# Optimization experiments

Measured on AMD Instinct MI355X. Metric: run time of the kernel, lower is better.

Reference implementation:

```python
import jax, jax.numpy as jnp
import numpy as np
from jax import lax

# SoftDTW constants from module-level `sdtw = SoftDTW(use_cuda=False, gamma=0.01, warp=134.4)`
GAMMA = 0.01
WARP = 134.4
BIG = 1e9        # finite stand-in for inf boundary (grad-safe; exp(-BIG/GAMMA) underflows to exactly 0)
MASK_INF = 100000.0
# loss alphas (config.loss.*)
KL_ALPHA = 1.0
KL_FWD_ALPHA = 1.0
GEN_ALPHA = 1.0
GEN_E2E_ALPHA = 1.0
FEAT_ALPHA = 2.0
DUR_ALPHA = 1.0
PITCH_ALPHA = 1.0
MEL_ALPHA = 45.0


def soft_dtw(D):
    """Soft-DTW with warp penalty (NaturalSpeech variant).
    D: [b, n, m] cost matrix. Returns [b] soft-DTW values R[n-1, m-1] of
      R[i,j] = D[i,j] + softmin_gamma(R[i-1,j-1], R[i-1,j]+warp, R[i,j-1]+warp)
    computed over anti-diagonals (wavefront) so each scan step is vectorized.
    """
    b, n, m = D.shape
    K = n + m - 1
    i_idx = jnp.arange(n)
    ks = jnp.arange(K)

    def pack(k):  # pack anti-diagonal k of D, indexed by row i
        j = k - i_idx
        v = (j >= 0) & (j < m)
        return jnp.where(v[None, :], D[:, i_idx, jnp.clip(j, 0, m - 1)], 0.0), v

    Dd, Vd = jax.vmap(pack)(ks)  # Dd: [K, b, n], Vd: [K, n]
    init = jnp.full((b, n), BIG, dtype=D.dtype)

    def step(carry, xs):
        r1, r2 = carry  # previous diag (k-1) and diag (k-2), indexed by row i
        dk, v, k = xs
        # diagonal predecessor (i-1, j-1): on diag k-2 at row i-1; (−1,−1) boundary = 0 only at k==0
        first = jnp.where(k == 0, 0.0, BIG).astype(D.dtype)
        r_diag = jnp.concatenate([jnp.broadcast_to(first, (b, 1)), r2[:, :-1]], axis=1)
        # up predecessor (i-1, j): diag k-1, row i-1
        r_up = jnp.concatenate([jnp.full((b, 1), BIG, dtype=D.dtype), r1[:, :-1]], axis=1)
        # left predecessor (i, j-1): diag k-1, row i
        stacked = jnp.stack([-r_diag, -(r_up + WARP), -(r1 + WARP)]) / GAMMA
        smin = -GAMMA * jax.nn.logsumexp(stacked, axis=0)
        r_new = jnp.where(v[None, :], dk + smin, BIG)
        return (r_new, r1), None

    (rf, _), _ = lax.scan(step, (init, init), (Dd, Vd, ks))
    return rf[:, n - 1]  # cell (n-1, m-1) lies on the last diagonal at row n-1


def kl_matrix(z, lq, m, lp):
    """kl[b,p,q] = sum_h lp - lq - 0.5 + 0.5*(z-m)^2*exp(-2lp); rows (m,lp) [b,h,P], cols (z,lq) [b,h,Q]."""
    h = m.shape[1]
    a = jnp.exp(-2.0 * lp)  # [b,h,P]
    quad = (jnp.einsum('bhp,bhq->bpq', a, z * z)
            - 2.0 * jnp.einsum('bhp,bhq->bpq', a * m, z)
            + jnp.sum(a * m * m, axis=1)[:, :, None])
    return jnp.sum(lp, axis=1)[:, :, None] - jnp.sum(lq, axis=1)[:, None, :] - 0.5 * h + 0.5 * quad


def kl_loss_sdtw(z, lq, m, lp, p_mask, q_mask):
    kl = kl_matrix(z, lq, m, lp)
    kl = jnp.pad(kl, ((0, 0), (0, 1), (0, 1)))
    pmf = jnp.pad(p_mask.astype(jnp.float32), ((0, 0), (0, 1)))
    qmf = jnp.pad(q_mask.astype(jnp.float32), ((0, 0), (0, 1)))
    pb, qb = pmf.astype(bool), qmf.astype(bool)
    kl = jnp.where(pb[:, :, None] ^ qb[:, None, :], MASK_INF, kl)
    kl = jnp.where((~pb[:, :, None]) & (~qb[:, None, :]), 0.0, kl)
    return soft_dtw(kl).sum() / pmf.sum()


def setup_inputs() -> dict:
    key = jax.random.key(0)
    ks = jax.random.split(key, 16)
    B, H, T = 8, 192, 400
    d = {
        'mel_slice': jax.random.normal(ks[0], (B, 80, T), jnp.float32),
        'mel_slice_hat': jax.random.normal(ks[1], (B, 80, T), jnp.float32),
        'scores_disc_fake': jax.random.normal(ks[2], (6, B, T), jnp.float32),
        'scores_disc_fake_e2e': jax.random.normal(ks[3], (6, B, T), jnp.float32),
        'feats_disc_real': jax.random.normal(ks[4], (30, B, 128, T), jnp.float32),
        'feats_disc_fake': jax.random.normal(ks[5], (30, B, 128, T), jnp.float32),
        'duration_loss': jax.random.uniform(ks[6], (1,), jnp.float32),
        'pitch_loss': jax.random.uniform(ks[7], (1,), jnp.float32),
        'z_p': jax.random.normal(ks[8], (B, H, T), jnp.float32),
        'm_p': jax.random.normal(ks[9], (B, H, T), jnp.float32),
        'logs_p': jax.random.normal(ks[10], (B, H, T), jnp.float32),
        'z_q': jax.random.normal(ks[11], (B, H, T), jnp.float32),
        'm_q': jax.random.normal(ks[12], (B, H, T), jnp.float32),
        'logs_q': jax.random.normal(ks[13], (B, H, T), jnp.float32),
        'p_mask': jnp.ones((B, T), jnp.int32),
        'z_mask': jnp.ones((B, T), jnp.int32),
    }
    return d


def reference(mel_slice, mel_slice_hat, scores_disc_fake, scores_disc_fake_e2e,
              feats_disc_real, feats_disc_fake, duration_loss, pitch_loss,
              z_p, m_p, logs_p, z_q, m_q, logs_q, p_mask, z_mask):
    # generator losses: sum over discriminator maps of mean((1 - s)^2)
    loss_gen = jnp.mean((1.0 - scores_disc_fake) ** 2, axis=(1, 2)).sum() * GEN_ALPHA
    loss_gen_e2e = jnp.mean((1.0 - scores_disc_fake_e2e) ** 2, axis=(1, 2)).sum() * GEN_E2E_ALPHA
    # feature matching: 2 * sum over feature maps of mean|real.detach() - fake|
    fr = lax.stop_gradient(feats_disc_real)
    loss_fm = 2.0 * jnp.mean(jnp.abs(fr - feats_disc_fake), axis=(1, 2, 3)).sum() * FEAT_ALPHA
    loss_mel = jnp.mean(jnp.abs(mel_slice - mel_slice_hat)) * MEL_ALPHA
    loss_dur = jnp.sum(duration_loss) * DUR_ALPHA
    loss_pitch = jnp.sum(pitch_loss) * PITCH_ALPHA
    # soft-DTW KL (both directions)
    loss_kl = kl_loss_sdtw(z_p, logs_q, m_p, logs_p, p_mask, z_mask) * KL_ALPHA
    loss_kl_fwd = kl_loss_sdtw(z_q, logs_p, m_q, logs_q, z_mask, p_mask) * KL_FWD_ALPHA
    total = loss_gen + loss_gen_e2e + loss_fm + loss_mel + loss_dur + loss_pitch + loss_kl + loss_kl_fwd
    return jnp.stack([loss_gen, loss_gen_e2e, loss_fm, loss_mel, loss_dur,
                      loss_pitch, loss_kl, loss_kl_fwd, total])
```

## Files before the change

### kernel.cpp

```cpp
#include <hip/hip_runtime.h>
#include <math.h>

#define BIGV      1e9f
#define WARP_PEN  134.4f
#define MASK_INF_C 100000.0f

#define B   8
#define H   192
#define T   400
#define NP  401
#define NPROB 16
#define TSLAB 166464
#define SBLOCKS 768

typedef float f32x4 __attribute__((ext_vector_type(4)));

#define SLOT_OFF 16
#define LSP_OFF 160
#define LSQ_OFF (160 + B*T)
#define C1P_OFF (160 + 2*B*T)
#define C1Q_OFF (160 + 3*B*T)
#define DMAT_OFF (160 + 4*B*T)

__device__ __forceinline__ int diag_len(int s) { return (s <= 50) ? s + 1 : 101 - s; }
__device__ __forceinline__ int diag_i0 (int s) { return (s <= 50) ? 0 : s - 50; }
__device__ __forceinline__ int diag_Cs (int s) {
    return (s <= 51) ? s * (s + 1) / 2 : 2601 - (101 - s) * (102 - s) / 2;
}

__device__ __forceinline__ float wave_shr1(float src, float fill) {
    int r = __builtin_amdgcn_update_dpp(__float_as_int(fill), __float_as_int(src),
                                        0x138 , 0xf, 0xf, false);
    return __int_as_float(r);
}

__global__ __launch_bounds__(256)
void colsum(const float* __restrict__ logs_p, const float* __restrict__ m_p,
            const float* __restrict__ logs_q, const float* __restrict__ m_q,
            float* __restrict__ ws) {
    int b = blockIdx.x / 7;
    int lane = threadIdx.x & 63;
    int hq = threadIdx.x >> 6;
    int t = (blockIdx.x % 7) * 64 + lane;
    __shared__ float part[4][4][64];
    float lp_s = 0.f, lq_s = 0.f, c1p = 0.f, c1q = 0.f;
    if (t < T) {
        int base = b*H*T + hq*48*T + t;
        const float* LP = logs_p + base;
        const float* MP = m_p   + base;
        const float* LQ = logs_q + base;
        const float* MQ = m_q   + base;
#pragma unroll 4
        for (int h = 0; h < 48; ++h) {
            float lp = LP[h*T], mp = MP[h*T];
            float lq = LQ[h*T], mq = MQ[h*T];
            lp_s += lp;
            lq_s += lq;
            c1p += __expf(-2.f*lp) * mp * mp;
            c1q += __expf(-2.f*lq) * mq * mq;
        }
    }
    part[hq][0][lane] = lp_s;
    part[hq][1][lane] = lq_s;
    part[hq][2][lane] = c1p;
    part[hq][3][lane] = c1q;
    __syncthreads();
    if (hq == 0 && t < T) {
        float a0 = part[0][0][lane] + part[1][0][lane] + part[2][0][lane] + part[3][0][lane];
        float a1 = part[0][1][lane] + part[1][1][lane] + part[2][1][lane] + part[3][1][lane];
        float a2 = part[0][2][lane] + part[1][2][lane] + part[2][2][lane] + part[3][2][lane];
        float a3 = part[0][3][lane] + part[1][3][lane] + part[2][3][lane] + part[3][3][lane];
        ws[LSP_OFF + b*T + t] = a0;
        ws[LSQ_OFF + b*T + t] = a1;
        ws[C1P_OFF + b*T + t] = a2;
        ws[C1Q_OFF + b*T + t] = a3;
    }
}

#define TILE 64
#define KH 32
__global__ __launch_bounds__(256)
void kl_gemm(const float* __restrict__ z_p, const float* __restrict__ m_p,
             const float* __restrict__ logs_p,
             const float* __restrict__ z_q, const float* __restrict__ m_q,
             const float* __restrict__ logs_q,
             const int* __restrict__ p_mask, const int* __restrict__ z_mask,
             float* __restrict__ ws) {
    int prob = blockIdx.y;
    int dir = prob >> 3, b = prob & 7;
    int tp = blockIdx.x / 7, tq = blockIdx.x % 7;
    int p0 = tp * TILE, q0 = tq * TILE;

    const float* lp_arr = dir ? logs_q : logs_p;
    const float* m_arr  = dir ? m_q    : m_p;
    const float* z_arr  = dir ? z_q    : z_p;
    const float* Lp = ws + (dir ? LSQ_OFF : LSP_OFF) + b*T;
    const float* Lq = ws + (dir ? LSP_OFF : LSQ_OFF) + b*T;
    const float* C1 = ws + (dir ? C1Q_OFF : C1P_OFF) + b*T;
    const int* rmask = dir ? z_mask : p_mask;
    const int* cmask = dir ? p_mask : z_mask;

    __shared__ __align__(16) float As [KH][TILE+4];
    __shared__ __align__(16) float AMs[KH][TILE+4];
    __shared__ __align__(16) float Zs [KH][TILE+4];
    __shared__ __align__(16) float Z2s[KH][TILE+4];

    int tid = threadIdx.x;
    int tx = tid & 15, ty = tid >> 4;

    float acc1[4][4] = {{0.f}}, acc2[4][4] = {{0.f}};

    const float* lpB = lp_arr + b*H*T;
    const float* mB  = m_arr  + b*H*T;
    const float* zB  = z_arr  + b*H*T;

    for (int h0 = 0; h0 < H; h0 += KH) {
        for (int e = tid; e < KH*TILE; e += 256) {
            int hh = e >> 6, tt = e & 63;
            int pg = p0 + tt; if (pg > T-1) pg = T-1;
            int qg = q0 + tt; if (qg > T-1) qg = T-1;
            float lp = lpB[(h0+hh)*T + pg];
            float mv = mB [(h0+hh)*T + pg];
            float a  = __expf(-2.f*lp);
            As [hh][tt] = a;
            AMs[hh][tt] = a * mv;
            float zv = zB[(h0+hh)*T + qg];
            Zs [hh][tt] = zv;
            Z2s[hh][tt] = zv * zv;
        }
        __syncthreads();
#pragma unroll 8
        for (int hh = 0; hh < KH; ++hh) {
            const float4 av  = *(const float4*)(&As [hh][ty*4]);
            const float4 amv = *(const float4*)(&AMs[hh][ty*4]);
            const float4 zv  = *(const float4*)(&Zs [hh][tx*4]);
            const float4 z2v = *(const float4*)(&Z2s[hh][tx*4]);
            const float pa[4]  = {av.x, av.y, av.z, av.w};
            const float pam[4] = {amv.x, amv.y, amv.z, amv.w};
            const float qz[4]  = {zv.x, zv.y, zv.z, zv.w};
            const float qz2[4] = {z2v.x, z2v.y, z2v.z, z2v.w};
#pragma unroll
            for (int ii = 0; ii < 4; ++ii)
#pragma unroll
                for (int jj = 0; jj < 4; ++jj) {
                    acc1[ii][jj] = fmaf(pa[ii],  qz2[jj], acc1[ii][jj]);
                    acc2[ii][jj] = fmaf(pam[ii], qz[jj],  acc2[ii][jj]);
                }
        }
        __syncthreads();
    }

    float* Dm = ws + DMAT_OFF + (size_t)prob * TSLAB;
#pragma unroll
    for (int ii = 0; ii < 4; ++ii) {
        int p = p0 + ty*4 + ii;
        if (p > NP-1) continue;
        int pc = p < T ? p : T-1;
        float lpv = Lp[pc];
        float c1v = C1[pc];
        bool pmv = (p < T) && (rmask[b*T + p] != 0);
#pragma unroll
        for (int jj = 0; jj < 4; ++jj) {
            int q = q0 + tx*4 + jj;
            if (q > NP-1) continue;
            int qc = q < T ? q : T-1;
            bool qmv = (q < T) && (cmask[b*T + q] != 0);
            float val = lpv - Lq[qc] - 0.5f*(float)H
                      + 0.5f*(acc1[ii][jj] - 2.f*acc2[ii][jj] + c1v);
            float outv = (pmv != qmv) ? MASK_INF_C : ((!pmv && !qmv) ? 0.f : val);
            int I8 = p >> 3, J8 = q >> 3, sdg = I8 + J8;
            int len = diag_len(sdg), i0 = diag_i0(sdg), Cs = diag_Cs(sdg);
            int k = (p & 7) * 2 + ((q & 7) >> 2);
            int off = Cs*64 + (k*len + (I8 - i0))*4 + (q & 3);
            Dm[off] = outv;
        }
    }
}

__global__ __launch_bounds__(256)
void fused_dtw_scalar(const float* __restrict__ Dd, float* __restrict__ acc,
                      const float* __restrict__ mel, const float* __restrict__ melh,
                      const float* __restrict__ sg,  const float* __restrict__ se,
                      const float* __restrict__ fr,  const float* __restrict__ ff,
                      const int* __restrict__ pm,    const int* __restrict__ zm) {
    if (blockIdx.x < NPROB) {
        if (threadIdx.x >= 64) return;
        int prob = blockIdx.x;
        int lane = threadIdx.x;
        const float* Dp = Dd + (size_t)prob * TSLAB;

        float brow[8], browW[8], rightraw[8], rightW[8];
        float brold = BIGV, v00 = BIGV;
#pragma unroll
        for (int t = 0; t < 8; ++t) {
            brow[t] = BIGV; browW[t] = BIGV; rightraw[t] = BIGV; rightW[t] = BIGV;
        }

        f32x4 bufA[16], bufB[16];

        auto load_diag = [&](int sp, f32x4* buf) {
            if (sp > 100) sp = 100;
            int len = diag_len(sp), i0 = diag_i0(sp), Cs = diag_Cs(sp);
            int pos = lane - i0;
            pos = pos < 0 ? 0 : pos;
            pos = pos > len - 1 ? len - 1 : pos;
            const float* srcb = Dp + Cs*64 + pos*4;
            int str = len * 4;
#pragma unroll
            for (int k = 0; k < 16; ++k)
                buf[k] = *(const f32x4*)(srcb + k*str);
        };

#define TILE_STEP(CUR, NXT, SVAL, DO_LOAD)                                    \
    {                                                                          \
        const int s_ = (SVAL);                                                 \
        bool jz = (s_ == lane);                                    \
        float brnew = brow[7];                                                 \
        _Pragma("unroll")                                                      \
        for (int c = 0; c < 8; ++c) {                                          \
            brow[c] = wave_shr1(brow[c], BIGV);                                \
            browW[c] = brow[c] + WARP_PEN;                                     \
        }                                                                      \
        float corner = wave_shr1(brold, BIGV);                                 \
        if (jz) corner = (lane == 0) ? 0.f : BIGV;                             \
        if (DO_LOAD) {                                                         \
            load_diag(s_ + 1, NXT);                                            \
            __builtin_amdgcn_sched_barrier(0);  \
        }                                                                      \
        float dprev = corner;                                                  \
        _Pragma("unroll")                                                      \
        for (int r = 0; r < 8; ++r) {                                          \
            float leftW = jz ? BIGV : rightW[r];                               \
            float dnextrow = jz ? BIGV : rightraw[r];                          \
            float diag = dprev;                                                \
            _Pragma("unroll")                                                  \
            for (int ch = 0; ch < 2; ++ch) {                                   \
                f32x4 dvv = CUR[r*2 + ch];                                     \
                _Pragma("unroll")                                              \
                for (int cc = 0; cc < 4; ++cc) {                               \
                    const int c = ch*4 + cc;                                   \
                    float v = fminf(fminf(diag, browW[c]), leftW) + dvv[cc];   \
                    if (r == 0 && c == 0) v00 = v;                             \
                    float t_ = brow[c];                                        \
                    brow[c] = v;                                               \
                    float vW = v + WARP_PEN;                                   \
                    browW[c] = vW;                                             \
                    leftW = vW;                                                \
                    diag = t_;                                                 \
                }                                                              \
            }                                                                  \
            rightraw[r] = brow[7];                                             \
            rightW[r]   = browW[7];                                            \
            dprev = dnextrow;                                                  \
        }                                                                      \
        brold = brnew;                                                         \
    }

        load_diag(0, bufA);

        for (int sb = 0; sb < 100; sb += 2) {
            TILE_STEP(bufA, bufB, sb,     1)
            TILE_STEP(bufB, bufA, sb + 1, 1)
        }
        TILE_STEP(bufA, bufB, 100, 0)
#undef TILE_STEP

        if (lane == 50) atomicAdd(&acc[6 + (prob >> 3)], v00);
    } else {
        float s0 = 0.f, s1 = 0.f, s2 = 0.f, s3 = 0.f, s4 = 0.f, s5 = 0.f;
        int tid = (blockIdx.x - NPROB) * 256 + threadIdx.x;
        const int stride = SBLOCKS * 256;

        const float4* fr4 = (const float4*)fr;
        const float4* ff4 = (const float4*)ff;
        for (int i = tid; i < 3072000; i += stride) {
            float4 a = fr4[i], b = ff4[i];
            s2 += fabsf(a.x - b.x) + fabsf(a.y - b.y) + fabsf(a.z - b.z) + fabsf(a.w - b.w);
        }
        const float4* m4 = (const float4*)mel;
        const float4* mh4 = (const float4*)melh;
        for (int i = tid; i < 64000; i += stride) {
            float4 a = m4[i], b = mh4[i];
            s3 += fabsf(a.x - b.x) + fabsf(a.y - b.y) + fabsf(a.z - b.z) + fabsf(a.w - b.w);
        }
        const float4* g4 = (const float4*)sg;
        const float4* e4 = (const float4*)se;
        for (int i = tid; i < 4800; i += stride) {
            float4 a = g4[i], b = e4[i];
            float gx = 1.f - a.x, gy = 1.f - a.y, gz = 1.f - a.z, gw = 1.f - a.w;
            s0 += gx*gx + gy*gy + gz*gz + gw*gw;
            float hx = 1.f - b.x, hy = 1.f - b.y, hz = 1.f - b.z, hw = 1.f - b.w;
            s1 += hx*hx + hy*hy + hz*hz + hw*hw;
        }
        for (int i = tid; i < B*T; i += stride) {
            s4 += (float)pm[i];
            s5 += (float)zm[i];
        }
        for (int off = 32; off > 0; off >>= 1) {
            s0 += __shfl_down(s0, off); s1 += __shfl_down(s1, off);
            s2 += __shfl_down(s2, off); s3 += __shfl_down(s3, off);
            s4 += __shfl_down(s4, off); s5 += __shfl_down(s5, off);
        }
        __shared__ float red[4][8];
        int wid = threadIdx.x >> 6;
        if ((threadIdx.x & 63) == 0) {
            red[wid][0] = s0; red[wid][1] = s1; red[wid][2] = s2;
            red[wid][3] = s3; red[wid][4] = s4; red[wid][5] = s5;
        }
        __syncthreads();
        if (threadIdx.x == 0) {
            float t0 = 0.f, t1 = 0.f, t2 = 0.f, t3 = 0.f, t4 = 0.f, t5 = 0.f;
#pragma unroll
            for (int w = 0; w < 4; ++w) {
                t0 += red[w][0]; t1 += red[w][1]; t2 += red[w][2];
                t3 += red[w][3]; t4 += red[w][4]; t5 += red[w][5];
            }
            float* slot = acc + SLOT_OFF + (blockIdx.x & 7) * 16;
            atomicAdd(&slot[0], t0); atomicAdd(&slot[1], t1);
            atomicAdd(&slot[2], t2); atomicAdd(&slot[3], t3);
            atomicAdd(&slot[4], t4); atomicAdd(&slot[5], t5);
        }
    }
}

__global__ void finalize(const float* __restrict__ acc,
                         const float* __restrict__ dur,
                         const float* __restrict__ pit,
                         float* __restrict__ out) {
    if (threadIdx.x != 0 || blockIdx.x != 0) return;
    float t[6] = {0.f, 0.f, 0.f, 0.f, 0.f, 0.f};
    for (int s = 0; s < 8; ++s)
        for (int c = 0; c < 6; ++c)
            t[c] += acc[SLOT_OFF + s*16 + c];
    float gen  = t[0] / 3200.f;
    float e2e  = t[1] / 3200.f;
    float fm   = 4.f * t[2] / 409600.f;
    float melv = 45.f * t[3] / 256000.f;
    float d    = dur[0];
    float p    = pit[0];
    float kl   = acc[6] / t[4];
    float klf  = acc[7] / t[5];
    out[0] = gen; out[1] = e2e; out[2] = fm; out[3] = melv;
    out[4] = d;   out[5] = p;   out[6] = kl; out[7] = klf;
    out[8] = gen + e2e + fm + melv + d + p + kl + klf;
}

extern "C" void kernel_launch(void* const* d_in, const int* in_sizes, int n_in,
                              void* d_out, int out_size, void* d_ws, size_t ws_size,
                              hipStream_t stream) {
    const float* mel    = (const float*)d_in[0];
    const float* melh   = (const float*)d_in[1];
    const float* sg     = (const float*)d_in[2];
    const float* se     = (const float*)d_in[3];
    const float* fr     = (const float*)d_in[4];
    const float* ff     = (const float*)d_in[5];
    const float* dur    = (const float*)d_in[6];
    const float* pit    = (const float*)d_in[7];
    const float* z_p    = (const float*)d_in[8];
    const float* m_p    = (const float*)d_in[9];
    const float* logs_p = (const float*)d_in[10];
    const float* z_q    = (const float*)d_in[11];
    const float* m_q    = (const float*)d_in[12];
    const float* logs_q = (const float*)d_in[13];
    const int*   p_mask = (const int*)d_in[14];
    const int*   z_mask = (const int*)d_in[15];
    float* ws  = (float*)d_ws;
    float* out = (float*)d_out;

    hipMemsetAsync(ws, 0, 160 * sizeof(float), stream);
    colsum<<<B*7, 256, 0, stream>>>(logs_p, m_p, logs_q, m_q, ws);
    kl_gemm<<<dim3(49, NPROB), 256, 0, stream>>>(z_p, m_p, logs_p, z_q, m_q, logs_q,
                                                 p_mask, z_mask, ws);
    fused_dtw_scalar<<<NPROB + SBLOCKS, 256, 0, stream>>>(ws + DMAT_OFF, ws,
                                                          mel, melh, sg, se, fr, ff,
                                                          p_mask, z_mask);
    finalize<<<1, 64, 0, stream>>>(ws, dur, pit, out);
}
```

Baseline: 145.1 us.

## Co-schedule scalar loss reductions with KL GEMM and run DTW separately

Moves the memory-bound feature/mel/generator reductions from the DTW kernel into the KL cost-matrix GEMM launch, so they overlap with the GEMM instead of with the serial soft-DTW wavefront. The DTW becomes its own 64-thread kernel with a one-wave launch bound. This hides the GEMM behind bandwidth-bound work, but the DTW's serial latency is no longer overlapped with anything.

```diff
diff --git a/kernel.cpp b/kernel.cpp
--- a/kernel.cpp
+++ b/kernel.cpp
@@ -12,6 +12,7 @@
 #define NPROB 16
 #define TSLAB 166464
 #define SBLOCKS 768
+#define KLBLOCKS (49 * NPROB)
 
 typedef float f32x4 __attribute__((ext_vector_type(4)));
 
@@ -80,136 +81,190 @@
 #define TILE 64
 #define KH 32
 __global__ __launch_bounds__(256)
-void kl_gemm(const float* __restrict__ z_p, const float* __restrict__ m_p,
-             const float* __restrict__ logs_p,
-             const float* __restrict__ z_q, const float* __restrict__ m_q,
-             const float* __restrict__ logs_q,
-             const int* __restrict__ p_mask, const int* __restrict__ z_mask,
-             float* __restrict__ ws) {
-    int prob = blockIdx.y;
-    int dir = prob >> 3, b = prob & 7;
-    int tp = blockIdx.x / 7, tq = blockIdx.x % 7;
-    int p0 = tp * TILE, q0 = tq * TILE;
-
-    const float* lp_arr = dir ? logs_q : logs_p;
-    const float* m_arr  = dir ? m_q    : m_p;
-    const float* z_arr  = dir ? z_q    : z_p;
-    const float* Lp = ws + (dir ? LSQ_OFF : LSP_OFF) + b*T;
-    const float* Lq = ws + (dir ? LSP_OFF : LSQ_OFF) + b*T;
-    const float* C1 = ws + (dir ? C1Q_OFF : C1P_OFF) + b*T;
-    const int* rmask = dir ? z_mask : p_mask;
-    const int* cmask = dir ? p_mask : z_mask;
-
+void fused_kl_scalar(const float* __restrict__ z_p, const float* __restrict__ m_p,
+                     const float* __restrict__ logs_p,
+                     const float* __restrict__ z_q, const float* __restrict__ m_q,
+                     const float* __restrict__ logs_q,
+                     const int* __restrict__ p_mask, const int* __restrict__ z_mask,
+                     float* __restrict__ ws,
+                     const float* __restrict__ mel, const float* __restrict__ melh,
+                     const float* __restrict__ sg,  const float* __restrict__ se,
+                     const float* __restrict__ fr,  const float* __restrict__ ff) {
     __shared__ __align__(16) float As [KH][TILE+4];
     __shared__ __align__(16) float AMs[KH][TILE+4];
     __shared__ __align__(16) float Zs [KH][TILE+4];
     __shared__ __align__(16) float Z2s[KH][TILE+4];
-
-    int tid = threadIdx.x;
-    int tx = tid & 15, ty = tid >> 4;
-
-    float acc1[4][4] = {{0.f}}, acc2[4][4] = {{0.f}};
-
-    const float* lpB = lp_arr + b*H*T;
-    const float* mB  = m_arr  + b*H*T;
-    const float* zB  = z_arr  + b*H*T;
-
-    for (int h0 = 0; h0 < H; h0 += KH) {
-        for (int e = tid; e < KH*TILE; e += 256) {
-            int hh = e >> 6, tt = e & 63;
-            int pg = p0 + tt; if (pg > T-1) pg = T-1;
-            int qg = q0 + tt; if (qg > T-1) qg = T-1;
-            float lp = lpB[(h0+hh)*T + pg];
-            float mv = mB [(h0+hh)*T + pg];
-            float a  = __expf(-2.f*lp);
-            As [hh][tt] = a;
-            AMs[hh][tt] = a * mv;
-            float zv = zB[(h0+hh)*T + qg];
-            Zs [hh][tt] = zv;
-            Z2s[hh][tt] = zv * zv;
+    __shared__ float red[4][8];
+
+    if (blockIdx.x < KLBLOCKS) {
+        int prob = blockIdx.x / 49;
+        int bx   = blockIdx.x % 49;
+        int dir = prob >> 3, b = prob & 7;
+        int tp = bx / 7, tq = bx % 7;
+        int p0 = tp * TILE, q0 = tq * TILE;
+
+        const float* lp_arr = dir ? logs_q : logs_p;
+        const float* m_arr  = dir ? m_q    : m_p;
+        const float* z_arr  = dir ? z_q    : z_p;
+        const float* Lp = ws + (dir ? LSQ_OFF : LSP_OFF) + b*T;
+        const float* Lq = ws + (dir ? LSP_OFF : LSQ_OFF) + b*T;
+        const float* C1 = ws + (dir ? C1Q_OFF : C1P_OFF) + b*T;
+        const int* rmask = dir ? z_mask : p_mask;
+        const int* cmask = dir ? p_mask : z_mask;
+
+        int tid = threadIdx.x;
+        int tx = tid & 15, ty = tid >> 4;
+
+        float acc1[4][4] = {{0.f}}, acc2[4][4] = {{0.f}};
+
+        const float* lpB = lp_arr + b*H*T;
+        const float* mB  = m_arr  + b*H*T;
+        const float* zB  = z_arr  + b*H*T;
+
+        for (int h0 = 0; h0 < H; h0 += KH) {
+            for (int e = tid; e < KH*TILE; e += 256) {
+                int hh = e >> 6, tt = e & 63;
+                int pg = p0 + tt; if (pg > T-1) pg = T-1;
+                int qg = q0 + tt; if (qg > T-1) qg = T-1;
+                float lp = lpB[(h0+hh)*T + pg];
+                float mv = mB [(h0+hh)*T + pg];
+                float a  = __expf(-2.f*lp);
+                As [hh][tt] = a;
+                AMs[hh][tt] = a * mv;
+                float zv = zB[(h0+hh)*T + qg];
+                Zs [hh][tt] = zv;
+                Z2s[hh][tt] = zv * zv;
+            }
+            __syncthreads();
+#pragma unroll 8
+            for (int hh = 0; hh < KH; ++hh) {
+                const float4 av  = *(const float4*)(&As [hh][ty*4]);
+                const float4 amv = *(const float4*)(&AMs[hh][ty*4]);
+                const float4 zv  = *(const float4*)(&Zs [hh][tx*4]);
+                const float4 z2v = *(const float4*)(&Z2s[hh][tx*4]);
+                const float pa[4]  = {av.x, av.y, av.z, av.w};
+                const float pam[4] = {amv.x, amv.y, amv.z, amv.w};
+                const float qz[4]  = {zv.x, zv.y, zv.z, zv.w};
+                const float qz2[4] = {z2v.x, z2v.y, z2v.z, z2v.w};
+#pragma unroll
+                for (int ii = 0; ii < 4; ++ii)
+#pragma unroll
+                    for (int jj = 0; jj < 4; ++jj) {
+                        acc1[ii][jj] = fmaf(pa[ii],  qz2[jj], acc1[ii][jj]);
+                        acc2[ii][jj] = fmaf(pam[ii], qz[jj],  acc2[ii][jj]);
+                    }
+            }
+            __syncthreads();
+        }
+
+        float* Dm = ws + DMAT_OFF + (size_t)prob * TSLAB;
+#pragma unroll
+        for (int ii = 0; ii < 4; ++ii) {
+            int p = p0 + ty*4 + ii;
+            if (p > NP-1) continue;
+            int pc = p < T ? p : T-1;
+            float lpv = Lp[pc];
+            float c1v = C1[pc];
+            bool pmv = (p < T) && (rmask[b*T + p] != 0);
+#pragma unroll
+            for (int jj = 0; jj < 4; ++jj) {
+                int q = q0 + tx*4 + jj;
+                if (q > NP-1) continue;
+                int qc = q < T ? q : T-1;
+                bool qmv = (q < T) && (cmask[b*T + q] != 0);
+                float val = lpv - Lq[qc] - 0.5f*(float)H
+                          + 0.5f*(acc1[ii][jj] - 2.f*acc2[ii][jj] + c1v);
+                float outv = (pmv != qmv) ? MASK_INF_C : ((!pmv && !qmv) ? 0.f : val);
+                int I8 = p >> 3, J8 = q >> 3, sdg = I8 + J8;
+                int len = diag_len(sdg), i0 = diag_i0(sdg), Cs = diag_Cs(sdg);
+                int k = (p & 7) * 2 + ((q & 7) >> 2);
+                int off = Cs*64 + (k*len + (I8 - i0))*4 + (q & 3);
+                Dm[off] = outv;
+            }
+        }
+    } else {
+        float s0 = 0.f, s1 = 0.f, s2 = 0.f, s3 = 0.f, s4 = 0.f, s5 = 0.f;
+        int tid = (blockIdx.x - KLBLOCKS) * 256 + threadIdx.x;
+        const int stride = SBLOCKS * 256;
+
+        const float4* fr4 = (const float4*)fr;
+        const float4* ff4 = (const float4*)ff;
+        for (int i = tid; i < 3072000; i += stride) {
+            float4 a = fr4[i], b = ff4[i];
+            s2 += fabsf(a.x - b.x) + fabsf(a.y - b.y) + fabsf(a.z - b.z) + fabsf(a.w - b.w);
+        }
+        const float4* m4 = (const float4*)mel;
+        const float4* mh4 = (const float4*)melh;
+        for (int i = tid; i < 64000; i += stride) {
+            float4 a = m4[i], b = mh4[i];
+            s3 += fabsf(a.x - b.x) + fabsf(a.y - b.y) + fabsf(a.z - b.z) + fabsf(a.w - b.w);
+        }
+        const float4* g4 = (const float4*)sg;
+        const float4* e4 = (const float4*)se;
+        for (int i = tid; i < 4800; i += stride) {
+            float4 a = g4[i], b = e4[i];
+            float gx = 1.f - a.x, gy = 1.f - a.y, gz = 1.f - a.z, gw = 1.f - a.w;
+            s0 += gx*gx + gy*gy + gz*gz + gw*gw;
+            float hx = 1.f - b.x, hy = 1.f - b.y, hz = 1.f - b.z, hw = 1.f - b.w;
+            s1 += hx*hx + hy*hy + hz*hz + hw*hw;
+        }
+        for (int i = tid; i < B*T; i += stride) {
+            s4 += (float)p_mask[i];
+            s5 += (float)z_mask[i];
+        }
+        for (int off = 32; off > 0; off >>= 1) {
+            s0 += __shfl_down(s0, off); s1 += __shfl_down(s1, off);
+            s2 += __shfl_down(s2, off); s3 += __shfl_down(s3, off);
+            s4 += __shfl_down(s4, off); s5 += __shfl_down(s5, off);
+        }
+        int wid = threadIdx.x >> 6;
+        if ((threadIdx.x & 63) == 0) {
+            red[wid][0] = s0; red[wid][1] = s1; red[wid][2] = s2;
+            red[wid][3] = s3; red[wid][4] = s4; red[wid][5] = s5;
         }
         __syncthreads();
-#pragma unroll 8
-        for (int hh = 0; hh < KH; ++hh) {
-            const float4 av  = *(const float4*)(&As [hh][ty*4]);
-            const float4 amv = *(const float4*)(&AMs[hh][ty*4]);
-            const float4 zv  = *(const float4*)(&Zs [hh][tx*4]);
-            const float4 z2v = *(const float4*)(&Z2s[hh][tx*4]);
-            const float pa[4]  = {av.x, av.y, av.z, av.w};
-            const float pam[4] = {amv.x, amv.y, amv.z, amv.w};
-            const float qz[4]  = {zv.x, zv.y, zv.z, zv.w};
-            const float qz2[4] = {z2v.x, z2v.y, z2v.z, z2v.w};
-#pragma unroll
-            for (int ii = 0; ii < 4; ++ii)
-#pragma unroll
-                for (int jj = 0; jj < 4; ++jj) {
-                    acc1[ii][jj] = fmaf(pa[ii],  qz2[jj], acc1[ii][jj]);
-                    acc2[ii][jj] = fmaf(pam[ii], qz[jj],  acc2[ii][jj]);
-                }
-        }
-        __syncthreads();
-    }
-
-    float* Dm = ws + DMAT_OFF + (size_t)prob * TSLAB;
-#pragma unroll
-    for (int ii = 0; ii < 4; ++ii) {
-        int p = p0 + ty*4 + ii;
-        if (p > NP-1) continue;
-        int pc = p < T ? p : T-1;
-        float lpv = Lp[pc];
-        float c1v = C1[pc];
-        bool pmv = (p < T) && (rmask[b*T + p] != 0);
-#pragma unroll
-        for (int jj = 0; jj < 4; ++jj) {
-            int q = q0 + tx*4 + jj;
-            if (q > NP-1) continue;
-            int qc = q < T ? q : T-1;
-            bool qmv = (q < T) && (cmask[b*T + q] != 0);
-            float val = lpv - Lq[qc] - 0.5f*(float)H
-                      + 0.5f*(acc1[ii][jj] - 2.f*acc2[ii][jj] + c1v);
-            float outv = (pmv != qmv) ? MASK_INF_C : ((!pmv && !qmv) ? 0.f : val);
-            int I8 = p >> 3, J8 = q >> 3, sdg = I8 + J8;
-            int len = diag_len(sdg), i0 = diag_i0(sdg), Cs = diag_Cs(sdg);
-            int k = (p & 7) * 2 + ((q & 7) >> 2);
-            int off = Cs*64 + (k*len + (I8 - i0))*4 + (q & 3);
-            Dm[off] = outv;
-        }
-    }
-}
-
-__global__ __launch_bounds__(256)
-void fused_dtw_scalar(const float* __restrict__ Dd, float* __restrict__ acc,
-                      const float* __restrict__ mel, const float* __restrict__ melh,
-                      const float* __restrict__ sg,  const float* __restrict__ se,
-                      const float* __restrict__ fr,  const float* __restrict__ ff,
-                      const int* __restrict__ pm,    const int* __restrict__ zm) {
-    if (blockIdx.x < NPROB) {
-        if (threadIdx.x >= 64) return;
-        int prob = blockIdx.x;
-        int lane = threadIdx.x;
-        const float* Dp = Dd + (size_t)prob * TSLAB;
-
-        float brow[8], browW[8], rightraw[8], rightW[8];
-        float brold = BIGV, v00 = BIGV;
-#pragma unroll
-        for (int t = 0; t < 8; ++t) {
-            brow[t] = BIGV; browW[t] = BIGV; rightraw[t] = BIGV; rightW[t] = BIGV;
-        }
-
-        f32x4 bufA[16], bufB[16];
-
-        auto load_diag = [&](int sp, f32x4* buf) {
-            if (sp > 100) sp = 100;
-            int len = diag_len(sp), i0 = diag_i0(sp), Cs = diag_Cs(sp);
-            int pos = lane - i0;
-            pos = pos < 0 ? 0 : pos;
-            pos = pos > len - 1 ? len - 1 : pos;
-            const float* srcb = Dp + Cs*64 + pos*4;
-            int str = len * 4;
-#pragma unroll
-            for (int k = 0; k < 16; ++k)
-                buf[k] = *(const f32x4*)(srcb + k*str);
-        };
+        if (threadIdx.x == 0) {
+            float t0 = 0.f, t1 = 0.f, t2 = 0.f, t3 = 0.f, t4 = 0.f, t5 = 0.f;
+#pragma unroll
+            for (int w = 0; w < 4; ++w) {
+                t0 += red[w][0]; t1 += red[w][1]; t2 += red[w][2];
+                t3 += red[w][3]; t4 += red[w][4]; t5 += red[w][5];
+            }
+            float* slot = ws + SLOT_OFF + (blockIdx.x & 7) * 16;
+            atomicAdd(&slot[0], t0); atomicAdd(&slot[1], t1);
+            atomicAdd(&slot[2], t2); atomicAdd(&slot[3], t3);
+            atomicAdd(&slot[4], t4); atomicAdd(&slot[5], t5);
+        }
+    }
+}
+
+__global__ __launch_bounds__(64, 1)
+void dtw_diag(const float* __restrict__ Dd, float* __restrict__ acc) {
+    int prob = blockIdx.x;
+    int lane = threadIdx.x;
+    const float* Dp = Dd + (size_t)prob * TSLAB;
+
+    float brow[8], browW[8], rightraw[8], rightW[8];
+    float brold = BIGV, v00 = BIGV;
+#pragma unroll
+    for (int t = 0; t < 8; ++t) {
+        brow[t] = BIGV; browW[t] = BIGV; rightraw[t] = BIGV; rightW[t] = BIGV;
+    }
+
+    f32x4 bufA[16], bufB[16];
+
+    auto load_diag = [&](int sp, f32x4* buf) {
+        if (sp > 100) sp = 100;
+        int len = diag_len(sp), i0 = diag_i0(sp), Cs = diag_Cs(sp);
+        int pos = lane - i0;
+        pos = pos < 0 ? 0 : pos;
+        pos = pos > len - 1 ? len - 1 : pos;
+        const float* srcb = Dp + Cs*64 + pos*4;
+        int str = len * 4;
+#pragma unroll
+        for (int k = 0; k < 16; ++k)
+            buf[k] = *(const f32x4*)(srcb + k*str);
+    };
 
 #define TILE_STEP(CUR, NXT, SVAL, DO_LOAD)                                    \
     {                                                                          \
@@ -256,71 +311,16 @@
         brold = brnew;                                                         \
     }
 
-        load_diag(0, bufA);
-
-        for (int sb = 0; sb < 100; sb += 2) {
-            TILE_STEP(bufA, bufB, sb,     1)
-            TILE_STEP(bufB, bufA, sb + 1, 1)
-        }
-        TILE_STEP(bufA, bufB, 100, 0)
+    load_diag(0, bufA);
+
+    for (int sb = 0; sb < 100; sb += 2) {
+        TILE_STEP(bufA, bufB, sb,     1)
+        TILE_STEP(bufB, bufA, sb + 1, 1)
+    }
+    TILE_STEP(bufA, bufB, 100, 0)
 #undef TILE_STEP
 
-        if (lane == 50) atomicAdd(&acc[6 + (prob >> 3)], v00);
-    } else {
-        float s0 = 0.f, s1 = 0.f, s2 = 0.f, s3 = 0.f, s4 = 0.f, s5 = 0.f;
-        int tid = (blockIdx.x - NPROB) * 256 + threadIdx.x;
-        const int stride = SBLOCKS * 256;
-
-        const float4* fr4 = (const float4*)fr;
-        const float4* ff4 = (const float4*)ff;
-        for (int i = tid; i < 3072000; i += stride) {
-            float4 a = fr4[i], b = ff4[i];
-            s2 += fabsf(a.x - b.x) + fabsf(a.y - b.y) + fabsf(a.z - b.z) + fabsf(a.w - b.w);
-        }
-        const float4* m4 = (const float4*)mel;
-        const float4* mh4 = (const float4*)melh;
-        for (int i = tid; i < 64000; i += stride) {
-            float4 a = m4[i], b = mh4[i];
-            s3 += fabsf(a.x - b.x) + fabsf(a.y - b.y) + fabsf(a.z - b.z) + fabsf(a.w - b.w);
-        }
-        const float4* g4 = (const float4*)sg;
-        const float4* e4 = (const float4*)se;
-        for (int i = tid; i < 4800; i += stride) {
-            float4 a = g4[i], b = e4[i];
-            float gx = 1.f - a.x, gy = 1.f - a.y, gz = 1.f - a.z, gw = 1.f - a.w;
-            s0 += gx*gx + gy*gy + gz*gz + gw*gw;
-            float hx = 1.f - b.x, hy = 1.f - b.y, hz = 1.f - b.z, hw = 1.f - b.w;
-            s1 += hx*hx + hy*hy + hz*hz + hw*hw;
-        }
-        for (int i = tid; i < B*T; i += stride) {
-            s4 += (float)pm[i];
-            s5 += (float)zm[i];
-        }
-        for (int off = 32; off > 0; off >>= 1) {
-            s0 += __shfl_down(s0, off); s1 += __shfl_down(s1, off);
-            s2 += __shfl_down(s2, off); s3 += __shfl_down(s3, off);
-            s4 += __shfl_down(s4, off); s5 += __shfl_down(s5, off);
-        }
-        __shared__ float red[4][8];
-        int wid = threadIdx.x >> 6;
-        if ((threadIdx.x & 63) == 0) {
-            red[wid][0] = s0; red[wid][1] = s1; red[wid][2] = s2;
-            red[wid][3] = s3; red[wid][4] = s4; red[wid][5] = s5;
-        }
-        __syncthreads();
-        if (threadIdx.x == 0) {
-            float t0 = 0.f, t1 = 0.f, t2 = 0.f, t3 = 0.f, t4 = 0.f, t5 = 0.f;
-#pragma unroll
-            for (int w = 0; w < 4; ++w) {
-                t0 += red[w][0]; t1 += red[w][1]; t2 += red[w][2];
-                t3 += red[w][3]; t4 += red[w][4]; t5 += red[w][5];
-            }
-            float* slot = acc + SLOT_OFF + (blockIdx.x & 7) * 16;
-            atomicAdd(&slot[0], t0); atomicAdd(&slot[1], t1);
-            atomicAdd(&slot[2], t2); atomicAdd(&slot[3], t3);
-            atomicAdd(&slot[4], t4); atomicAdd(&slot[5], t5);
-        }
-    }
+    if (lane == 50) atomicAdd(&acc[6 + (prob >> 3)], v00);
 }
 
 __global__ void finalize(const float* __restrict__ acc,
@@ -369,10 +369,9 @@
 
     hipMemsetAsync(ws, 0, 160 * sizeof(float), stream);
     colsum<<<B*7, 256, 0, stream>>>(logs_p, m_p, logs_q, m_q, ws);
-    kl_gemm<<<dim3(49, NPROB), 256, 0, stream>>>(z_p, m_p, logs_p, z_q, m_q, logs_q,
-                                                 p_mask, z_mask, ws);
-    fused_dtw_scalar<<<NPROB + SBLOCKS, 256, 0, stream>>>(ws + DMAT_OFF, ws,
-                                                          mel, melh, sg, se, fr, ff,
-                                                          p_mask, z_mask);
+    fused_kl_scalar<<<KLBLOCKS + SBLOCKS, 256, 0, stream>>>(
+        z_p, m_p, logs_p, z_q, m_q, logs_q, p_mask, z_mask, ws,
+        mel, melh, sg, se, fr, ff);
+    dtw_diag<<<NPROB, 64, 0, stream>>>(ws + DMAT_OFF, ws);
     finalize<<<1, 64, 0, stream>>>(ws, dur, pit, out);
 }
```

New measurement: 141.6 us. 2.4% less time.
